# Kernel tuning notes

Hardware: AMD Instinct MI355X
Metric: run time of the kernel (lower is better)

## Reference

```python
import math
import jax, jax.numpy as jnp
import numpy as np

B, S, H = 8, 2048, 1024
NH = 1
DH = H // NH          # head dim == hidden since NH=1 (required by module's math)
DT = 64               # distance_type


def setup_inputs() -> dict:
    key = jax.random.key(0)
    ks = jax.random.split(key, 10)
    hidden_states = jax.random.normal(ks[0], (B, S, H), dtype=jnp.float32)
    attention_mask = jnp.zeros((B, 1, 1, S), dtype=jnp.float32)
    word_word_relation = jax.random.randint(ks[1], (B, S, S), 0, DT, dtype=jnp.int32)
    init = 0.02
    Wq = jax.random.normal(ks[2], (H, H), dtype=jnp.float32) * init
    bq = jnp.zeros((H,), dtype=jnp.float32)
    Wk = jax.random.normal(ks[3], (H, H), dtype=jnp.float32) * init
    bk = jnp.zeros((H,), dtype=jnp.float32)
    Wv = jax.random.normal(ks[4], (H, H), dtype=jnp.float32) * init
    bv = jnp.zeros((H,), dtype=jnp.float32)
    dist_emb = jax.random.normal(ks[5], (DT, H), dtype=jnp.float32) * init
    dist_emb = dist_emb.at[0].set(0.0)  # padding_idx=0
    return {
        "hidden_states": hidden_states,
        "attention_mask": attention_mask,
        "word_word_relation": word_word_relation,
        "Wq": Wq, "bq": bq, "Wk": Wk, "bk": bk, "Wv": Wv, "bv": bv,
        "dist_emb": dist_emb,
    }


def reference(hidden_states, attention_mask, word_word_relation,
              Wq, bq, Wk, bk, Wv, bv, dist_emb):
    b, s, h = hidden_states.shape
    def heads(x):  # [b,s,h] -> [b,nh,s,dh]
        return x.reshape(b, s, NH, DH).transpose(0, 2, 1, 3)
    q = heads(hidden_states @ Wq.T + bq)
    k = heads(hidden_states @ Wk.T + bk)
    v = heads(hidden_states @ Wv.T + bv)

    scores = jnp.einsum('bhqd,bhkd->bhqk', q, k)                 # [b,nh,s,s]
    word_dot_distance = jnp.einsum('bhqd,td->bhqt', q, dist_emb) # [b,nh,s,DT]

    idx = word_word_relation[:, None, :, :]                      # [b,1,s,s]
    bias = jnp.take_along_axis(word_dot_distance, idx, axis=3)
    mask_out = (word_word_relation == 1)[:, None].astype(scores.dtype)
    bias = bias * mask_out

    scores = (scores + bias) / math.sqrt(DH) + attention_mask
    probs = jax.nn.softmax(scores, axis=-1)
    ctx = jnp.einsum('bhqk,bhkd->bhqd', probs, v)
    ctx = ctx.transpose(0, 2, 1, 3).reshape(b, s, h)
    return ctx
```

## Files before the change

kernel.cpp:

```cpp
#include <hip/hip_runtime.h>

typedef unsigned short u16;
typedef __bf16 bf16x8 __attribute__((ext_vector_type(8)));
typedef u16 u16x8 __attribute__((ext_vector_type(8)));
typedef float f32x4 __attribute__((ext_vector_type(4)));

#define S_LEN 2048
#define H_LEN 1024

__device__ __forceinline__ u16 f2b(float f) {
  unsigned u = __float_as_uint(f);
  return (u16)((u + 0x7FFFu + ((u >> 16) & 1u)) >> 16);
}
__device__ __forceinline__ float b2f(u16 h) { return __uint_as_float(((unsigned)h) << 16); }

#define GLOAD16(gp, lp)                                   \
  __builtin_amdgcn_global_load_lds(                       \
      (__attribute__((address_space(1))) void*)(gp),      \
      (__attribute__((address_space(3))) void*)(lp), 16, 0, 0)

__global__ __launch_bounds__(256) void prep_kernel(
    const float* __restrict__ X, const float* __restrict__ Wq,
    const float* __restrict__ Wk, const float* __restrict__ Wv,
    const float* __restrict__ bq, const float* __restrict__ bk,
    const float* __restrict__ bv, const float* __restrict__ dist,
    const int* __restrict__ rel,
    u16* __restrict__ Xbf, u16* __restrict__ Wbf, float* __restrict__ b_all,
    u16* __restrict__ de1, unsigned* __restrict__ bits, float* __restrict__ d1) {
  size_t tid = (size_t)blockIdx.x * blockDim.x + threadIdx.x;
  size_t nth = (size_t)gridDim.x * blockDim.x;
  for (size_t i = tid; i < 4194304u; i += nth) {
    float4 v = ((const float4*)X)[i];
    ushort4 o; o.x = f2b(v.x); o.y = f2b(v.y); o.z = f2b(v.z); o.w = f2b(v.w);
    ((ushort4*)Xbf)[i] = o;
  }
  for (size_t i = tid; i < 786432u; i += nth) {
    int which = (int)(i >> 18);
    size_t off = i & 262143u;
    const float4* src = (const float4*)(which == 0 ? Wq : (which == 1 ? Wk : Wv));
    float4 v = src[off];
    ushort4 o; o.x = f2b(v.x); o.y = f2b(v.y); o.z = f2b(v.z); o.w = f2b(v.w);
    ((ushort4*)Wbf)[i] = o;
  }
  const int4* r4 = (const int4*)rel;
  for (size_t wi = tid; wi < 1048576u; wi += nth) {
    const int4* s = r4 + wi * 8;
    unsigned m = 0;
#pragma unroll
    for (int u = 0; u < 8; ++u) {
      int4 v = s[u];
      m |= (unsigned)(v.x == 1) << (u * 4 + 0);
      m |= (unsigned)(v.y == 1) << (u * 4 + 1);
      m |= (unsigned)(v.z == 1) << (u * 4 + 2);
      m |= (unsigned)(v.w == 1) << (u * 4 + 3);
    }
    bits[wi] = m;
  }
  for (size_t i = tid; i < 256u; i += nth) {
    float4 v = ((const float4*)(dist + H_LEN))[i];
    ushort4 o; o.x = f2b(v.x); o.y = f2b(v.y); o.z = f2b(v.z); o.w = f2b(v.w);
    ((ushort4*)de1)[i] = o;
  }
  for (size_t i = tid; i < 3072u; i += nth)
    b_all[i] = (i < 1024) ? bq[i] : (i < 2048 ? bk[i - 1024] : bv[i - 2048]);
  for (size_t i = tid; i < 16384u; i += nth) d1[i] = 0.f;
}

struct GArgs {
  const u16* A; const u16* B;
  long long sA, sB;
  int ldA, ldB, K;
  u16 *Qo, *Ko, *Vo; const float* b_all; const u16* de1; float* d1;
  const unsigned* relbits; const float* mask; u16* P;
  float* outp;
};

template <int EPI>
__global__ __launch_bounds__(256) void gemm_nt(GArgs g) {
  const int bz = blockIdx.z;
  int bx = blockIdx.x, by = blockIdx.y;
  if constexpr (EPI == 0) {
    const int lin = by * 24 + bx;
    const int band = lin / (24 * 8), rem = lin % (24 * 8);
    by = band * 8 + (rem & 7);
    bx = rem >> 3;
  }
  const u16* Abase = g.A + (size_t)bz * g.sA;
  const u16* Bbase = g.B + (size_t)bz * g.sB;
  const int m0 = by * 128, n0 = bx * 128;

  __shared__ u16 smem[16384];
  u16* As = smem;
  u16* Bs = smem + 8192;

  const int tid = threadIdx.x;
  const int lane = tid & 63, w = tid >> 6;
  const int wm = w >> 1, wn = w & 1;
  const int l15 = lane & 15, quad = lane >> 4;

  f32x4 acc[4][4];
  f32x4 acc_sum[4];
  const f32x4 zero = {0.f, 0.f, 0.f, 0.f};
#pragma unroll
  for (int a = 0; a < 4; ++a) {
    acc_sum[a] = zero;
#pragma unroll
    for (int b = 0; b < 4; ++b) acc[a][b] = zero;
  }
  bf16x8 ones;
#pragma unroll
  for (int i = 0; i < 8; ++i) ones[i] = (__bf16)1.0f;

  const int c0 = tid, c1 = tid + 256;
  const u16* ga0 = Abase + (size_t)(m0 + (c0 >> 2)) * g.ldA + (c0 & 3) * 8;
  const u16* ga1 = Abase + (size_t)(m0 + (c1 >> 2)) * g.ldA + (c1 & 3) * 8;
  const u16* gb0 = Bbase + (size_t)(n0 + (c0 >> 2)) * g.ldB + (c0 & 3) * 8;
  const u16* gb1 = Bbase + (size_t)(n0 + (c1 >> 2)) * g.ldB + (c1 & 3) * 8;
  u16* la0 = As + c0 * 8; u16* la1 = As + c1 * 8;
  u16* lb0 = Bs + c0 * 8; u16* lb1 = Bs + c1 * 8;

  for (int kt = 0; kt < g.K; kt += 64) {
    __syncthreads();
    GLOAD16(ga0 + kt, la0);      GLOAD16(ga0 + kt + 32, la0 + 4096);
    GLOAD16(ga1 + kt, la1);      GLOAD16(ga1 + kt + 32, la1 + 4096);
    GLOAD16(gb0 + kt, lb0);      GLOAD16(gb0 + kt + 32, lb0 + 4096);
    GLOAD16(gb1 + kt, lb1);      GLOAD16(gb1 + kt + 32, lb1 + 4096);
    __syncthreads();
#pragma unroll
    for (int s = 0; s < 2; ++s) {
      bf16x8 af[4], bfb[4];
#pragma unroll
      for (int t = 0; t < 4; ++t) {
        af[t]  = *(const bf16x8*)&As[s * 4096 + (wm * 64 + t * 16 + l15) * 32 + quad * 8];
        bfb[t] = *(const bf16x8*)&Bs[s * 4096 + (wn * 64 + t * 16 + l15) * 32 + quad * 8];
      }
#pragma unroll
      for (int mt = 0; mt < 4; ++mt) {
#pragma unroll
        for (int nt = 0; nt < 4; ++nt)
          acc[mt][nt] = __builtin_amdgcn_mfma_f32_16x16x32_bf16(af[mt], bfb[nt], acc[mt][nt], 0, 0, 0);
        if constexpr (EPI == 2)
          acc_sum[mt] = __builtin_amdgcn_mfma_f32_16x16x32_bf16(af[mt], ones, acc_sum[mt], 0, 0, 0);
      }
    }
  }
  __syncthreads();

  const int nbase = n0 + wn * 64;

  if constexpr (EPI == 0) {
    const int which = n0 >> 10;
    float bv4[4], dw[4];
#pragma unroll
    for (int nt = 0; nt < 4; ++nt) {
      bv4[nt] = g.b_all[nbase + nt * 16 + l15];
      dw[nt] = (which == 0) ? b2f(g.de1[nbase + nt * 16 + l15]) : 0.f;
    }
#pragma unroll
    for (int mt = 0; mt < 4; ++mt)
#pragma unroll
      for (int r = 0; r < 4; ++r) {
        const int row = wm * 64 + mt * 16 + quad * 4 + r;
        float part = 0.f;
#pragma unroll
        for (int nt = 0; nt < 4; ++nt) {
          const float v = acc[mt][nt][r] + bv4[nt];
          part += v * dw[nt];
          const int col = wn * 64 + nt * 16 + l15;
          const int chunkS = (col >> 3) ^ (row & 15);
          smem[row * 128 + chunkS * 8 + (col & 7)] = f2b(v);
        }
        if (which == 0) {
          part += __shfl_xor(part, 1);
          part += __shfl_xor(part, 2);
          part += __shfl_xor(part, 4);
          part += __shfl_xor(part, 8);
          if (l15 == 0) atomicAdd(&g.d1[m0 + row], part);
        }
      }
    __syncthreads();
    u16* dstbuf = which == 0 ? g.Qo : (which == 1 ? g.Ko : g.Vo);
    const int nl0 = n0 & 1023;
#pragma unroll
    for (int p = 0; p < 8; ++p) {
      const int flat = p * 256 + tid;
      const int row = flat >> 4, chunk = flat & 15;
      const int chunkS = chunk ^ (row & 15);
      u16x8 v = *(const u16x8*)&smem[row * 128 + chunkS * 8];
      *(u16x8*)(dstbuf + (size_t)(m0 + row) * H_LEN + nl0 + chunk * 8) = v;
    }
  }

  if constexpr (EPI == 1) {
    float mk[4];
#pragma unroll
    for (int nt = 0; nt < 4; ++nt) mk[nt] = g.mask[bz * S_LEN + nbase + nt * 16 + l15];
    const size_t bSS = (size_t)bz * S_LEN * S_LEN;
#pragma unroll
    for (int mt = 0; mt < 4; ++mt)
#pragma unroll
      for (int r = 0; r < 4; ++r) {
        const int row = wm * 64 + mt * 16 + quad * 4 + r;
        const int gi = bz * S_LEN + m0 + row;
        const float d1v = g.d1[gi] * 0.03125f;
        const unsigned w0 = g.relbits[(size_t)gi * 64 + (nbase >> 5)];
        const unsigned w1 = g.relbits[(size_t)gi * 64 + (nbase >> 5) + 1];
#pragma unroll
        for (int nt = 0; nt < 4; ++nt) {
          const unsigned word = (nt & 2) ? w1 : w0;
          const int pos = (nt * 16 + l15) & 31;
          const float bias = ((word >> pos) & 1) ? d1v : 0.f;
          const float logit = acc[mt][nt][r] * 0.03125f + bias + mk[nt];
          const float pv = __expf(logit);
          const int col = wn * 64 + nt * 16 + l15;
          const int chunkS = (col >> 3) ^ (row & 15);
          smem[row * 128 + chunkS * 8 + (col & 7)] = f2b(pv);
        }
      }
    __syncthreads();
#pragma unroll
    for (int p = 0; p < 8; ++p) {
      const int flat = p * 256 + tid;
      const int row = flat >> 4, chunk = flat & 15;
      const int chunkS = chunk ^ (row & 15);
      u16x8 v = *(const u16x8*)&smem[row * 128 + chunkS * 8];
      *(u16x8*)(g.P + bSS + (size_t)(m0 + row) * S_LEN + n0 + chunk * 8) = v;
    }
  }

  if constexpr (EPI == 2) {
    const size_t ob = (size_t)bz * S_LEN * H_LEN;
#pragma unroll
    for (int mt = 0; mt < 4; ++mt)
#pragma unroll
      for (int r = 0; r < 4; ++r) {
        const int i = m0 + wm * 64 + mt * 16 + quad * 4 + r;
        const float inv = 1.0f / acc_sum[mt][r];
        const size_t rowo = ob + (size_t)i * H_LEN;
#pragma unroll
        for (int nt = 0; nt < 4; ++nt) {
          const int d = n0 + wn * 64 + nt * 16 + l15;
          g.outp[rowo + d] = acc[mt][nt][r] * inv;
        }
      }
  }
}

__global__ __launch_bounds__(256) void transpose_v(const u16* __restrict__ V,
                                                   u16* __restrict__ Vt) {
  const int b = blockIdx.z;
  const int j0 = blockIdx.x * 64;
  const int d0 = blockIdx.y * 64;
  __shared__ u16 t[64][72];
  const int tid = threadIdx.x;
  const int tr = tid >> 4;
  const int tc = (tid & 15) * 4;
#pragma unroll
  for (int p = 0; p < 4; ++p) {
    const int jl = p * 16 + tr;
    const u16* src = V + ((size_t)b * S_LEN + (j0 + jl)) * H_LEN + d0 + tc;
    ushort4 v = *(const ushort4*)src;
    t[jl][tc + 0] = v.x; t[jl][tc + 1] = v.y; t[jl][tc + 2] = v.z; t[jl][tc + 3] = v.w;
  }
  __syncthreads();
#pragma unroll
  for (int p = 0; p < 4; ++p) {
    const int dl = p * 16 + tr;
    ushort4 v;
    v.x = t[tc + 0][dl]; v.y = t[tc + 1][dl]; v.z = t[tc + 2][dl]; v.w = t[tc + 3][dl];
    *(ushort4*)(Vt + ((size_t)b * H_LEN + (d0 + dl)) * S_LEN + j0 + tc) = v;
  }
}

extern "C" void kernel_launch(void* const* d_in, const int* in_sizes, int n_in,
                              void* d_out, int out_size, void* d_ws, size_t ws_size,
                              hipStream_t stream) {
  (void)in_sizes; (void)n_in; (void)out_size; (void)ws_size;
  const float* X    = (const float*)d_in[0];
  const float* mask = (const float*)d_in[1];
  const int*   rel  = (const int*)d_in[2];
  const float* Wq   = (const float*)d_in[3];
  const float* bq   = (const float*)d_in[4];
  const float* Wk   = (const float*)d_in[5];
  const float* bk   = (const float*)d_in[6];
  const float* Wv   = (const float*)d_in[7];
  const float* bv   = (const float*)d_in[8];
  const float* dist = (const float*)d_in[9];
  float* out = (float*)d_out;

  char* p = (char*)d_ws;
  u16* Xbf = (u16*)p;      p += (size_t)16384 * 1024 * 2;
  u16* Wbf = (u16*)p;      p += (size_t)3072 * 1024 * 2;
  float* b_all = (float*)p; p += 3072 * 4;
  u16* de1 = (u16*)p;      p += 4096;
  u16* Qb = (u16*)p;       p += (size_t)16384 * 1024 * 2;
  u16* Kb = (u16*)p;       p += (size_t)16384 * 1024 * 2;
  u16* Vb = (u16*)p;       p += (size_t)16384 * 1024 * 2;
  u16* Vt = (u16*)p;       p += (size_t)16384 * 1024 * 2;
  float* d1 = (float*)p;   p += 16384 * 4;
  unsigned* relbits = (unsigned*)p; p += (size_t)1048576 * 4;
  u16* P = (u16*)p;        p += (size_t)8 * 2048 * 2048 * 2;

  prep_kernel<<<1024, 256, 0, stream>>>(X, Wq, Wk, Wv, bq, bk, bv, dist, rel,
                                        Xbf, Wbf, b_all, de1, relbits, d1);

  GArgs g0 = {};
  g0.A = Xbf; g0.B = Wbf; g0.sA = 0; g0.sB = 0;
  g0.ldA = 1024; g0.ldB = 1024; g0.K = 1024;
  g0.Qo = Qb; g0.Ko = Kb; g0.Vo = Vb; g0.b_all = b_all; g0.de1 = de1; g0.d1 = d1;
  gemm_nt<0><<<dim3(24, 128, 1), dim3(256, 1, 1), 0, stream>>>(g0);

  transpose_v<<<dim3(32, 16, 8), dim3(256, 1, 1), 0, stream>>>(Vb, Vt);

  GArgs g1 = {};
  g1.A = Qb; g1.B = Kb; g1.sA = 2048LL * 1024; g1.sB = 2048LL * 1024;
  g1.ldA = 1024; g1.ldB = 1024; g1.K = 1024;
  g1.relbits = relbits; g1.d1 = d1; g1.mask = mask; g1.P = P;
  gemm_nt<1><<<dim3(16, 16, 8), dim3(256, 1, 1), 0, stream>>>(g1);

  GArgs g2 = {};
  g2.A = P; g2.B = Vt; g2.sA = 2048LL * 2048; g2.sB = 1024LL * 2048;
  g2.ldA = 2048; g2.ldB = 2048; g2.K = 2048;
  g2.outp = out;
  gemm_nt<2><<<dim3(8, 16, 8), dim3(256, 1, 1), 0, stream>>>(g2);
}
```

Measured before the change: 642.5 us.

## Replace 128x128 GEMM with double-buffered 256x256 tile kernel and precomputed softmax denominators

Replaces the 128x128 single-buffered GEMM with a 256x256-tile, 512-thread kernel. The new kernel double-buffers K-slices in LDS, swizzles the LDS layout, interleaves MFMA phases with barriers and priority hints, and waits on vmcnt explicitly. The softmax denominator is now accumulated with atomics in the QK epilogue from the rounded bf16 probabilities, instead of an extra ones-vector MFMA in the PV GEMM. The aim is more data reuse per tile and hiding load latency behind compute, at the cost of higher register and LDS use and fewer workgroups for the smaller grids.

Measured after the change: 611.7 us. 1.05x faster.

```diff
diff --git a/kernel.cpp b/kernel.cpp
--- a/kernel.cpp
+++ b/kernel.cpp
@@ -18,6 +18,24 @@
   __builtin_amdgcn_global_load_lds(                       \
       (__attribute__((address_space(1))) void*)(gp),      \
       (__attribute__((address_space(3))) void*)(lp), 16, 0, 0)
+
+#define FENCE() asm volatile("" ::: "memory")
+#define PBAR()                           \
+  do {                                   \
+    FENCE();                             \
+    __builtin_amdgcn_s_barrier();        \
+    FENCE();                             \
+  } while (0)
+#define WAIT_LGKM0()                                        \
+  do {                                                      \
+    asm volatile("s_waitcnt lgkmcnt(0)" ::: "memory");      \
+    __builtin_amdgcn_sched_barrier(0);                      \
+  } while (0)
+#define WAIT_VM(n) asm volatile("s_waitcnt vmcnt(" #n ")" ::: "memory")
+
+__device__ __forceinline__ f32x4 MM(bf16x8 a, bf16x8 b, f32x4 c) {
+  return __builtin_amdgcn_mfma_f32_16x16x32_bf16(a, b, c, 0, 0, 0);
+}
 
 __global__ __launch_bounds__(256) void prep_kernel(
     const float* __restrict__ X, const float* __restrict__ Wq,
@@ -63,7 +81,7 @@
   }
   for (size_t i = tid; i < 3072u; i += nth)
     b_all[i] = (i < 1024) ? bq[i] : (i < 2048 ? bk[i - 1024] : bv[i - 2048]);
-  for (size_t i = tid; i < 16384u; i += nth) d1[i] = 0.f;
+  for (size_t i = tid; i < 32768u; i += nth) d1[i] = 0.f;
 }
 
 struct GArgs {
@@ -71,104 +89,181 @@
   long long sA, sB;
   int ldA, ldB, K;
   u16 *Qo, *Ko, *Vo; const float* b_all; const u16* de1; float* d1;
-  const unsigned* relbits; const float* mask; u16* P;
+  const unsigned* relbits; const float* mask; u16* P; float* denom;
   float* outp;
 };
 
 template <int EPI>
-__global__ __launch_bounds__(256) void gemm_nt(GArgs g) {
+__global__ __launch_bounds__(512, 2) void gemm256(GArgs g) {
   const int bz = blockIdx.z;
   int bx = blockIdx.x, by = blockIdx.y;
   if constexpr (EPI == 0) {
-    const int lin = by * 24 + bx;
-    const int band = lin / (24 * 8), rem = lin % (24 * 8);
-    by = band * 8 + (rem & 7);
-    bx = rem >> 3;
+    const int lin = bx;
+    const int wg = (lin & 7) * 96 + (lin >> 3);
+    by = wg / 12; bx = wg % 12;
   }
   const u16* Abase = g.A + (size_t)bz * g.sA;
   const u16* Bbase = g.B + (size_t)bz * g.sB;
-  const int m0 = by * 128, n0 = bx * 128;
-
-  __shared__ u16 smem[16384];
-  u16* As = smem;
-  u16* Bs = smem + 8192;
+  const int m0 = by * 256, n0 = bx * 256;
+
+  __shared__ u16 smem[65536];
 
   const int tid = threadIdx.x;
   const int lane = tid & 63, w = tid >> 6;
-  const int wm = w >> 1, wn = w & 1;
+  const int wm = w >> 2, wn = w & 3;
   const int l15 = lane & 15, quad = lane >> 4;
 
-  f32x4 acc[4][4];
-  f32x4 acc_sum[4];
+  f32x4 acc[8][4];
   const f32x4 zero = {0.f, 0.f, 0.f, 0.f};
 #pragma unroll
-  for (int a = 0; a < 4; ++a) {
-    acc_sum[a] = zero;
+  for (int a = 0; a < 8; ++a)
 #pragma unroll
     for (int b = 0; b < 4; ++b) acc[a][b] = zero;
-  }
-  bf16x8 ones;
-#pragma unroll
-  for (int i = 0; i < 8; ++i) ones[i] = (__bf16)1.0f;
-
-  const int c0 = tid, c1 = tid + 256;
-  const u16* ga0 = Abase + (size_t)(m0 + (c0 >> 2)) * g.ldA + (c0 & 3) * 8;
-  const u16* ga1 = Abase + (size_t)(m0 + (c1 >> 2)) * g.ldA + (c1 & 3) * 8;
-  const u16* gb0 = Bbase + (size_t)(n0 + (c0 >> 2)) * g.ldB + (c0 & 3) * 8;
-  const u16* gb1 = Bbase + (size_t)(n0 + (c1 >> 2)) * g.ldB + (c1 & 3) * 8;
-  u16* la0 = As + c0 * 8; u16* la1 = As + c1 * 8;
-  u16* lb0 = Bs + c0 * 8; u16* lb1 = Bs + c1 * 8;
-
-  for (int kt = 0; kt < g.K; kt += 64) {
-    __syncthreads();
-    GLOAD16(ga0 + kt, la0);      GLOAD16(ga0 + kt + 32, la0 + 4096);
-    GLOAD16(ga1 + kt, la1);      GLOAD16(ga1 + kt + 32, la1 + 4096);
-    GLOAD16(gb0 + kt, lb0);      GLOAD16(gb0 + kt + 32, lb0 + 4096);
-    GLOAD16(gb1 + kt, lb1);      GLOAD16(gb1 + kt + 32, lb1 + 4096);
-    __syncthreads();
-#pragma unroll
-    for (int s = 0; s < 2; ++s) {
-      bf16x8 af[4], bfb[4];
-#pragma unroll
-      for (int t = 0; t < 4; ++t) {
-        af[t]  = *(const bf16x8*)&As[s * 4096 + (wm * 64 + t * 16 + l15) * 32 + quad * 8];
-        bfb[t] = *(const bf16x8*)&Bs[s * 4096 + (wn * 64 + t * 16 + l15) * 32 + quad * 8];
-      }
-#pragma unroll
-      for (int mt = 0; mt < 4; ++mt) {
-#pragma unroll
-        for (int nt = 0; nt < 4; ++nt)
-          acc[mt][nt] = __builtin_amdgcn_mfma_f32_16x16x32_bf16(af[mt], bfb[nt], acc[mt][nt], 0, 0, 0);
-        if constexpr (EPI == 2)
-          acc_sum[mt] = __builtin_amdgcn_mfma_f32_16x16x32_bf16(af[mt], ones, acc_sum[mt], 0, 0, 0);
-      }
-    }
-  }
-  __syncthreads();
+
+  const u16* gA[4]; const u16* gB[4]; int qoff[4];
+#pragma unroll
+  for (int r = 0; r < 4; ++r) {
+    const int q = r * 512 + tid;
+    const int row = q >> 3, ch = q & 7;
+    const int chS = ch ^ (row & 7);
+    gA[r] = Abase + (size_t)(m0 + row) * g.ldA + chS * 8;
+    gB[r] = Bbase + (size_t)(n0 + row) * g.ldB + chS * 8;
+    qoff[r] = q * 8;
+  }
+
+  auto stage = [&](int boff2, int kt) {
+#pragma unroll
+    for (int r = 0; r < 4; ++r) GLOAD16(gA[r] + kt, &smem[boff2 + qoff[r]]);
+#pragma unroll
+    for (int r = 0; r < 4; ++r) GLOAD16(gB[r] + kt, &smem[boff2 + 16384 + qoff[r]]);
+  };
+
+  const int NT = g.K >> 6;
+
+  stage(0, 0);
+  stage(32768, 64);
+  WAIT_VM(8);
+  PBAR();
+
+  bf16x8 af[4][2], bfr[4][2];
+
+  for (int t = 0; t < NT; ++t) {
+    const int boff = (t & 1) << 15;
+    const u16* Ab = smem + boff;
+    const u16* Bb = smem + boff + 16384;
+
+#pragma unroll
+    for (int mt = 0; mt < 4; ++mt) {
+      const int row = wm * 128 + mt * 16 + l15;
+      const int base = row * 64, rx = row & 7;
+      af[mt][0] = *(const bf16x8*)&Ab[base + ((quad ^ rx) << 3)];
+      af[mt][1] = *(const bf16x8*)&Ab[base + (((quad + 4) ^ rx) << 3)];
+    }
+#pragma unroll
+    for (int nt = 0; nt < 2; ++nt) {
+      const int row = wn * 64 + nt * 16 + l15;
+      const int base = row * 64, rx = row & 7;
+      bfr[nt][0] = *(const bf16x8*)&Bb[base + ((quad ^ rx) << 3)];
+      bfr[nt][1] = *(const bf16x8*)&Bb[base + (((quad + 4) ^ rx) << 3)];
+    }
+    PBAR();
+    WAIT_LGKM0();
+    __builtin_amdgcn_s_setprio(1);
+#pragma unroll
+    for (int mt = 0; mt < 4; ++mt)
+#pragma unroll
+      for (int nt = 0; nt < 2; ++nt) {
+        acc[mt][nt] = MM(af[mt][0], bfr[nt][0], acc[mt][nt]);
+        acc[mt][nt] = MM(af[mt][1], bfr[nt][1], acc[mt][nt]);
+      }
+    __builtin_amdgcn_s_setprio(0);
+    PBAR();
+
+#pragma unroll
+    for (int nt = 2; nt < 4; ++nt) {
+      const int row = wn * 64 + nt * 16 + l15;
+      const int base = row * 64, rx = row & 7;
+      bfr[nt][0] = *(const bf16x8*)&Bb[base + ((quad ^ rx) << 3)];
+      bfr[nt][1] = *(const bf16x8*)&Bb[base + (((quad + 4) ^ rx) << 3)];
+    }
+    PBAR();
+    WAIT_LGKM0();
+    __builtin_amdgcn_s_setprio(1);
+#pragma unroll
+    for (int mt = 0; mt < 4; ++mt)
+#pragma unroll
+      for (int nt = 2; nt < 4; ++nt) {
+        acc[mt][nt] = MM(af[mt][0], bfr[nt][0], acc[mt][nt]);
+        acc[mt][nt] = MM(af[mt][1], bfr[nt][1], acc[mt][nt]);
+      }
+    __builtin_amdgcn_s_setprio(0);
+    PBAR();
+
+#pragma unroll
+    for (int mt = 0; mt < 4; ++mt) {
+      const int row = wm * 128 + (mt + 4) * 16 + l15;
+      const int base = row * 64, rx = row & 7;
+      af[mt][0] = *(const bf16x8*)&Ab[base + ((quad ^ rx) << 3)];
+      af[mt][1] = *(const bf16x8*)&Ab[base + (((quad + 4) ^ rx) << 3)];
+    }
+    PBAR();
+    WAIT_LGKM0();
+    __builtin_amdgcn_s_setprio(1);
+#pragma unroll
+    for (int mt = 0; mt < 4; ++mt)
+#pragma unroll
+      for (int nt = 0; nt < 2; ++nt) {
+        acc[mt + 4][nt] = MM(af[mt][0], bfr[nt][0], acc[mt + 4][nt]);
+        acc[mt + 4][nt] = MM(af[mt][1], bfr[nt][1], acc[mt + 4][nt]);
+      }
+    __builtin_amdgcn_s_setprio(0);
+    PBAR();
+
+    if (t + 2 < NT) stage(boff, (t + 2) << 6);
+    PBAR();
+    WAIT_LGKM0();
+    __builtin_amdgcn_s_setprio(1);
+#pragma unroll
+    for (int mt = 0; mt < 4; ++mt)
+#pragma unroll
+      for (int nt = 2; nt < 4; ++nt) {
+        acc[mt + 4][nt] = MM(af[mt][0], bfr[nt][0], acc[mt + 4][nt]);
+        acc[mt + 4][nt] = MM(af[mt][1], bfr[nt][1], acc[mt + 4][nt]);
+      }
+    __builtin_amdgcn_s_setprio(0);
+    if (t + 2 < NT) {
+      WAIT_VM(8);
+    } else if (t + 1 < NT) {
+      WAIT_VM(0);
+    }
+    PBAR();
+  }
 
   const int nbase = n0 + wn * 64;
 
   if constexpr (EPI == 0) {
     const int which = n0 >> 10;
+    const int nl0 = n0 & 1023;
     float bv4[4], dw[4];
 #pragma unroll
     for (int nt = 0; nt < 4; ++nt) {
-      bv4[nt] = g.b_all[nbase + nt * 16 + l15];
-      dw[nt] = (which == 0) ? b2f(g.de1[nbase + nt * 16 + l15]) : 0.f;
-    }
-#pragma unroll
-    for (int mt = 0; mt < 4; ++mt)
+      const int col = wn * 64 + nt * 16 + l15;
+      bv4[nt] = g.b_all[n0 + col];
+      dw[nt] = (which == 0) ? b2f(g.de1[nl0 + col]) : 0.f;
+    }
+#pragma unroll
+    for (int mt = 0; mt < 8; ++mt)
 #pragma unroll
       for (int r = 0; r < 4; ++r) {
-        const int row = wm * 64 + mt * 16 + quad * 4 + r;
+        const int row = wm * 128 + mt * 16 + quad * 4 + r;
         float part = 0.f;
 #pragma unroll
         for (int nt = 0; nt < 4; ++nt) {
           const float v = acc[mt][nt][r] + bv4[nt];
           part += v * dw[nt];
           const int col = wn * 64 + nt * 16 + l15;
-          const int chunkS = (col >> 3) ^ (row & 15);
-          smem[row * 128 + chunkS * 8 + (col & 7)] = f2b(v);
+          const int chS = (col >> 3) ^ (row & 31);
+          smem[row * 256 + chS * 8 + (col & 7)] = f2b(v);
         }
         if (which == 0) {
           part += __shfl_xor(part, 1);
@@ -180,13 +275,12 @@
       }
     __syncthreads();
     u16* dstbuf = which == 0 ? g.Qo : (which == 1 ? g.Ko : g.Vo);
-    const int nl0 = n0 & 1023;
-#pragma unroll
-    for (int p = 0; p < 8; ++p) {
-      const int flat = p * 256 + tid;
-      const int row = flat >> 4, chunk = flat & 15;
-      const int chunkS = chunk ^ (row & 15);
-      u16x8 v = *(const u16x8*)&smem[row * 128 + chunkS * 8];
+#pragma unroll
+    for (int p = 0; p < 16; ++p) {
+      const int flat = p * 512 + tid;
+      const int row = flat >> 5, chunk = flat & 31;
+      const int chS = chunk ^ (row & 31);
+      u16x8 v = *(const u16x8*)&smem[row * 256 + chS * 8];
       *(u16x8*)(dstbuf + (size_t)(m0 + row) * H_LEN + nl0 + chunk * 8) = v;
     }
   }
@@ -196,15 +290,17 @@
 #pragma unroll
     for (int nt = 0; nt < 4; ++nt) mk[nt] = g.mask[bz * S_LEN + nbase + nt * 16 + l15];
     const size_t bSS = (size_t)bz * S_LEN * S_LEN;
-#pragma unroll
-    for (int mt = 0; mt < 4; ++mt)
+    const int wbase = (n0 + wn * 64) >> 5;
+#pragma unroll
+    for (int mt = 0; mt < 8; ++mt)
 #pragma unroll
       for (int r = 0; r < 4; ++r) {
-        const int row = wm * 64 + mt * 16 + quad * 4 + r;
+        const int row = wm * 128 + mt * 16 + quad * 4 + r;
         const int gi = bz * S_LEN + m0 + row;
         const float d1v = g.d1[gi] * 0.03125f;
-        const unsigned w0 = g.relbits[(size_t)gi * 64 + (nbase >> 5)];
-        const unsigned w1 = g.relbits[(size_t)gi * 64 + (nbase >> 5) + 1];
+        const unsigned w0 = g.relbits[(size_t)gi * 64 + wbase];
+        const unsigned w1 = g.relbits[(size_t)gi * 64 + wbase + 1];
+        float dsum = 0.f;
 #pragma unroll
         for (int nt = 0; nt < 4; ++nt) {
           const unsigned word = (nt & 2) ? w1 : w0;
@@ -212,18 +308,25 @@
           const float bias = ((word >> pos) & 1) ? d1v : 0.f;
           const float logit = acc[mt][nt][r] * 0.03125f + bias + mk[nt];
           const float pv = __expf(logit);
+          const u16 pb = f2b(pv);
+          dsum += b2f(pb);
           const int col = wn * 64 + nt * 16 + l15;
-          const int chunkS = (col >> 3) ^ (row & 15);
-          smem[row * 128 + chunkS * 8 + (col & 7)] = f2b(pv);
+          const int chS = (col >> 3) ^ (row & 31);
+          smem[row * 256 + chS * 8 + (col & 7)] = pb;
         }
+        dsum += __shfl_xor(dsum, 1);
+        dsum += __shfl_xor(dsum, 2);
+        dsum += __shfl_xor(dsum, 4);
+        dsum += __shfl_xor(dsum, 8);
+        if (l15 == 0) atomicAdd(&g.denom[gi], dsum);
       }
     __syncthreads();
 #pragma unroll
-    for (int p = 0; p < 8; ++p) {
-      const int flat = p * 256 + tid;
-      const int row = flat >> 4, chunk = flat & 15;
-      const int chunkS = chunk ^ (row & 15);
-      u16x8 v = *(const u16x8*)&smem[row * 128 + chunkS * 8];
+    for (int p = 0; p < 16; ++p) {
+      const int flat = p * 512 + tid;
+      const int row = flat >> 5, chunk = flat & 31;
+      const int chS = chunk ^ (row & 31);
+      u16x8 v = *(const u16x8*)&smem[row * 256 + chS * 8];
       *(u16x8*)(g.P + bSS + (size_t)(m0 + row) * S_LEN + n0 + chunk * 8) = v;
     }
   }
@@ -231,17 +334,15 @@
   if constexpr (EPI == 2) {
     const size_t ob = (size_t)bz * S_LEN * H_LEN;
 #pragma unroll
-    for (int mt = 0; mt < 4; ++mt)
+    for (int mt = 0; mt < 8; ++mt)
 #pragma unroll
       for (int r = 0; r < 4; ++r) {
-        const int i = m0 + wm * 64 + mt * 16 + quad * 4 + r;
-        const float inv = 1.0f / acc_sum[mt][r];
-        const size_t rowo = ob + (size_t)i * H_LEN;
-#pragma unroll
-        for (int nt = 0; nt < 4; ++nt) {
-          const int d = n0 + wn * 64 + nt * 16 + l15;
-          g.outp[rowo + d] = acc[mt][nt][r] * inv;
-        }
+        const int row = wm * 128 + mt * 16 + quad * 4 + r;
+        const float inv = 1.0f / g.denom[bz * S_LEN + m0 + row];
+        const size_t rowo = ob + (size_t)(m0 + row) * H_LEN;
+#pragma unroll
+        for (int nt = 0; nt < 4; ++nt)
+          g.outp[rowo + nbase + nt * 16 + l15] = acc[mt][nt][r] * inv;
       }
   }
 }
@@ -298,6 +399,7 @@
   u16* Vb = (u16*)p;       p += (size_t)16384 * 1024 * 2;
   u16* Vt = (u16*)p;       p += (size_t)16384 * 1024 * 2;
   float* d1 = (float*)p;   p += 16384 * 4;
+  float* denom = (float*)p; p += 16384 * 4;
   unsigned* relbits = (unsigned*)p; p += (size_t)1048576 * 4;
   u16* P = (u16*)p;        p += (size_t)8 * 2048 * 2048 * 2;
 
@@ -308,19 +410,19 @@
   g0.A = Xbf; g0.B = Wbf; g0.sA = 0; g0.sB = 0;
   g0.ldA = 1024; g0.ldB = 1024; g0.K = 1024;
   g0.Qo = Qb; g0.Ko = Kb; g0.Vo = Vb; g0.b_all = b_all; g0.de1 = de1; g0.d1 = d1;
-  gemm_nt<0><<<dim3(24, 128, 1), dim3(256, 1, 1), 0, stream>>>(g0);
+  gemm256<0><<<dim3(768, 1, 1), dim3(512, 1, 1), 0, stream>>>(g0);
 
   transpose_v<<<dim3(32, 16, 8), dim3(256, 1, 1), 0, stream>>>(Vb, Vt);
 
   GArgs g1 = {};
   g1.A = Qb; g1.B = Kb; g1.sA = 2048LL * 1024; g1.sB = 2048LL * 1024;
   g1.ldA = 1024; g1.ldB = 1024; g1.K = 1024;
-  g1.relbits = relbits; g1.d1 = d1; g1.mask = mask; g1.P = P;
-  gemm_nt<1><<<dim3(16, 16, 8), dim3(256, 1, 1), 0, stream>>>(g1);
+  g1.relbits = relbits; g1.d1 = d1; g1.mask = mask; g1.P = P; g1.denom = denom;
+  gemm256<1><<<dim3(8, 8, 8), dim3(512, 1, 1), 0, stream>>>(g1);
 
   GArgs g2 = {};
   g2.A = P; g2.B = Vt; g2.sA = 2048LL * 2048; g2.sB = 1024LL * 2048;
   g2.ldA = 2048; g2.ldB = 2048; g2.K = 2048;
-  g2.outp = out;
-  gemm_nt<2><<<dim3(8, 16, 8), dim3(256, 1, 1), 0, stream>>>(g2);
-}
+  g2.denom = denom; g2.outp = out;
+  gemm256<2><<<dim3(4, 8, 8), dim3(512, 1, 1), 0, stream>>>(g2);
+}
```
